# Performance work log

Hardware: AMD Instinct MI355X
Metric: run time of the kernel (lower is better)

The kernel has to match this reference:

```python
import jax, jax.numpy as jnp
import numpy as np

N_MASTER = 100000
N_BOND = 200000
N_GLOB = 5000
E1 = 400000
E2 = 100000
D_IN = 64
D_OUT = 64
H = 4
SLOPE = 0.2  # leaky relu negative slope


def _mlp(x, W0, b0, W1, b1, W2):
    # LinearN with num_fc_layers=3: ELU, ELU, Identity (last layer no bias)
    h = jax.nn.elu(x @ W0 + b0)
    h = jax.nn.elu(h @ W1 + b1)
    return h @ W2  # (N, H*D_OUT)


def setup_inputs() -> dict:
    key = jax.random.key(0)
    ks = jax.random.split(key, 32)
    s = 0.1  # weight scale
    d = {
        "master_feats": jax.random.normal(ks[0], (N_MASTER, D_IN), jnp.float32),
        "bond_feats": jax.random.normal(ks[1], (N_BOND, D_IN), jnp.float32),
        "global_feats": jax.random.normal(ks[2], (N_GLOB, D_IN), jnp.float32),
        "atom_W0": jax.random.normal(ks[3], (D_IN, D_OUT), jnp.float32) * s,
        "atom_b0": jnp.zeros((D_OUT,), jnp.float32),
        "atom_W1": jax.random.normal(ks[4], (D_OUT, D_OUT), jnp.float32) * s,
        "atom_b1": jnp.zeros((D_OUT,), jnp.float32),
        "atom_W2": jax.random.normal(ks[5], (D_OUT, H * D_OUT), jnp.float32) * s,
        "bond_W0": jax.random.normal(ks[6], (D_IN, D_OUT), jnp.float32) * s,
        "bond_b0": jnp.zeros((D_OUT,), jnp.float32),
        "bond_W1": jax.random.normal(ks[7], (D_OUT, D_OUT), jnp.float32) * s,
        "bond_b1": jnp.zeros((D_OUT,), jnp.float32),
        "bond_W2": jax.random.normal(ks[8], (D_OUT, H * D_OUT), jnp.float32) * s,
        "glob_W0": jax.random.normal(ks[9], (D_IN, D_OUT), jnp.float32) * s,
        "glob_b0": jnp.zeros((D_OUT,), jnp.float32),
        "glob_W1": jax.random.normal(ks[10], (D_OUT, D_OUT), jnp.float32) * s,
        "glob_b1": jnp.zeros((D_OUT,), jnp.float32),
        "glob_W2": jax.random.normal(ks[11], (D_OUT, H * D_OUT), jnp.float32) * s,
        "attn_l": jax.random.normal(ks[12], (H, D_OUT), jnp.float32) * s,
        "attn_r": jax.random.normal(ks[13], (H, D_OUT), jnp.float32) * s,
        "e1_src": jax.random.randint(ks[14], (E1,), 0, N_BOND, jnp.int32),
        "e1_dst": jax.random.randint(ks[15], (E1,), 0, N_MASTER, jnp.int32),
        "e2_src": jax.random.randint(ks[16], (E2,), 0, N_GLOB, jnp.int32),
        "e2_dst": jax.random.randint(ks[17], (E2,), 0, N_MASTER, jnp.int32),
    }
    return d


def reference(master_feats, bond_feats, global_feats,
              atom_W0, atom_b0, atom_W1, atom_b1, atom_W2,
              bond_W0, bond_b0, bond_W1, bond_b1, bond_W2,
              glob_W0, glob_b0, glob_W1, glob_b1, glob_W2,
              attn_l, attn_r, e1_src, e1_dst, e2_src, e2_dst):
    # Per-node-type projections to (N, H, D_OUT)
    ft_m = _mlp(master_feats, atom_W0, atom_b0, atom_W1, atom_b1, atom_W2).reshape(N_MASTER, H, D_OUT)
    ft_b = _mlp(bond_feats, bond_W0, bond_b0, bond_W1, bond_b1, bond_W2).reshape(N_BOND, H, D_OUT)
    ft_g = _mlp(global_feats, glob_W0, glob_b0, glob_W1, glob_b1, glob_W2).reshape(N_GLOB, H, D_OUT)

    er = jnp.einsum('nhd,hd->nh', ft_m, attn_r)  # master (dst) scores
    el_b = jnp.einsum('nhd,hd->nh', ft_b, attn_l)
    el_g = jnp.einsum('nhd,hd->nh', ft_g, attn_l)

    # Per-edge logits: u_add_v then leaky relu
    e1 = jax.nn.leaky_relu(el_b[e1_src] + er[e1_dst], negative_slope=SLOPE)  # (E1, H)
    e2 = jax.nn.leaky_relu(el_g[e2_src] + er[e2_dst], negative_slope=SLOPE)  # (E2, H)

    # Joint edge softmax over all incoming edges per master node
    dst_all = jnp.concatenate([e1_dst, e2_dst])  # (E1+E2,)
    e_all = jnp.concatenate([e1, e2], axis=0)    # (E1+E2, H)
    emax = jax.ops.segment_max(e_all, dst_all, num_segments=N_MASTER)  # (N, H)
    ex = jnp.exp(e_all - emax[dst_all])
    esum = jax.ops.segment_sum(ex, dst_all, num_segments=N_MASTER)     # (N, H)
    a = ex / esum[dst_all]                                             # (E, H)

    # Aggregate: u_mul_e, sum per destination master node
    src_ft = jnp.concatenate([ft_b[e1_src], ft_g[e2_src]], axis=0)     # (E, H, D)
    msgs = src_ft * a[:, :, None]
    rst = jax.ops.segment_sum(msgs, dst_all, num_segments=N_MASTER)    # (N, H, D)
    return rst
```

## Files before the change

kernel.cpp:

```cpp
#include <hip/hip_runtime.h>

#define NM 100000
#define NB 200000
#define NG 5000
#define NE1 400000
#define NE2 100000
#define NE (NE1 + NE2)
#define NMP 100004
#define SCAN_BLOCKS 391

typedef __attribute__((ext_vector_type(8))) short bf16x8;
typedef __attribute__((ext_vector_type(4))) short short4v;
typedef __attribute__((ext_vector_type(4))) float f32x4;

__device__ __forceinline__ unsigned short f2bf(float f) {
    unsigned int u = __float_as_uint(f);
    u += 0x7FFFu + ((u >> 16) & 1u);
    return (unsigned short)(u >> 16);
}
__device__ __forceinline__ float bf2f(unsigned short u) {
    return __uint_as_float((unsigned int)u << 16);
}
__device__ __forceinline__ float elu_f(float x) {
    return x > 0.f ? x : __expf(x) - 1.f;
}
__device__ __forceinline__ char* swz(char* base, int j, int byteoff) {
    return base + j * 128 + ((((byteoff >> 4) ^ (j & 7)) << 4) | (byteoff & 15));
}

struct WEnt { const float* W; short* o; int I; int off; };
struct WAll { WEnt e[9]; };

__global__ __launch_bounds__(256) void wprep_all_kernel(WAll a)
{
    const int idx = blockIdx.x * 256 + threadIdx.x;
    #pragma unroll
    for (int j = 8; j >= 0; --j) {
        if (idx >= a.e[j].off) {
            const int local = idx - a.e[j].off;
            const int I = a.e[j].I;
            const int i = local >> 6, k = local & 63;
            a.e[j].o[local] = (short)f2bf(a.e[j].W[k * I + i]);
            break;
        }
    }
}

__global__ __launch_bounds__(256) void mlp_mfma_kernel(
    const float* __restrict__ x, int N,
    const short* __restrict__ W0t, const float* __restrict__ b0,
    const short* __restrict__ W1t, const float* __restrict__ b1,
    const short* __restrict__ W2t,
    const float* __restrict__ attn,
    float* __restrict__ score,
    unsigned short* __restrict__ ft_out)
{
    __shared__ __attribute__((aligned(128))) char ldsA[64 * 128];
    __shared__ __attribute__((aligned(128))) char ldsB[64 * 128];

    const int tid = threadIdx.x;
    const int w = tid >> 6, l = tid & 63;
    const int g = l >> 4, c = l & 15;
    const int r0 = blockIdx.x << 6;

    {
        const int j = tid >> 2, q = tid & 3;
        const int row = r0 + j;
        bf16x8 o0 = (bf16x8)0, o1 = (bf16x8)0;
        if (row < N) {
            const float4* xp = (const float4*)(x + ((size_t)row << 6) + (q << 4));
            #pragma unroll
            for (int u = 0; u < 2; ++u) {
                float4 v = xp[u];
                o0[u*4+0] = (short)f2bf(v.x); o0[u*4+1] = (short)f2bf(v.y);
                o0[u*4+2] = (short)f2bf(v.z); o0[u*4+3] = (short)f2bf(v.w);
            }
            #pragma unroll
            for (int u = 0; u < 2; ++u) {
                float4 v = xp[u + 2];
                o1[u*4+0] = (short)f2bf(v.x); o1[u*4+1] = (short)f2bf(v.y);
                o1[u*4+2] = (short)f2bf(v.z); o1[u*4+3] = (short)f2bf(v.w);
            }
        }
        *(bf16x8*)swz(ldsA, j, q * 32)      = o0;
        *(bf16x8*)swz(ldsA, j, q * 32 + 16) = o1;
    }
    __syncthreads();

    char* src = ldsA;
    char* dst = ldsB;
    #pragma unroll
    for (int layer = 0; layer < 2; ++layer) {
        const short* Wt = layer ? W1t : W0t;
        const float* bb = layer ? b1 : b0;
        f32x4 acc[4] = {};
        #pragma unroll
        for (int step = 0; step < 2; ++step) {
            bf16x8 a = *(const bf16x8*)(Wt + (((16 * w + c) << 6) + 32 * step + 8 * g));
            #pragma unroll
            for (int t = 0; t < 4; ++t) {
                const int j = 16 * t + c;
                bf16x8 b = *(const bf16x8*)swz(src, j, 64 * step + 16 * g);
                acc[t] = __builtin_amdgcn_mfma_f32_16x16x32_bf16(a, b, acc[t], 0, 0, 0);
            }
        }
        const int i0 = 16 * w + 4 * g;
        const float4 bias = *(const float4*)(bb + i0);
        #pragma unroll
        for (int t = 0; t < 4; ++t) {
            const int j = 16 * t + c;
            short4v o;
            o[0] = (short)f2bf(elu_f(acc[t][0] + bias.x));
            o[1] = (short)f2bf(elu_f(acc[t][1] + bias.y));
            o[2] = (short)f2bf(elu_f(acc[t][2] + bias.z));
            o[3] = (short)f2bf(elu_f(acc[t][3] + bias.w));
            *(short4v*)swz(dst, j, 32 * w + 8 * g) = o;
        }
        __syncthreads();
        char* tmp = src; src = dst; dst = tmp;
    }

    {
        f32x4 acc[4][4] = {};
        #pragma unroll
        for (int step = 0; step < 2; ++step) {
            bf16x8 bfr[4];
            #pragma unroll
            for (int t = 0; t < 4; ++t)
                bfr[t] = *(const bf16x8*)swz(src, 16 * t + c, 64 * step + 16 * g);
            #pragma unroll
            for (int it = 0; it < 4; ++it) {
                bf16x8 a = *(const bf16x8*)(W2t + (((64 * w + 16 * it + c) << 6) + 32 * step + 8 * g));
                #pragma unroll
                for (int t = 0; t < 4; ++t)
                    acc[it][t] = __builtin_amdgcn_mfma_f32_16x16x32_bf16(a, bfr[t], acc[it][t], 0, 0, 0);
            }
        }
        float4 av[4];
        #pragma unroll
        for (int it = 0; it < 4; ++it)
            av[it] = *(const float4*)(attn + 64 * w + 16 * it + 4 * g);

        #pragma unroll
        for (int t = 0; t < 4; ++t) {
            const int row = r0 + 16 * t + c;
            float p = 0.f;
            #pragma unroll
            for (int it = 0; it < 4; ++it) {
                p += acc[it][t][0] * av[it].x + acc[it][t][1] * av[it].y
                   + acc[it][t][2] * av[it].z + acc[it][t][3] * av[it].w;
            }
            p += __shfl_xor(p, 16);
            p += __shfl_xor(p, 32);
            if (row < N) {
                if (g == 0) score[(row << 2) + w] = p;
                if (ft_out) {
                    #pragma unroll
                    for (int it = 0; it < 4; ++it) {
                        short4v o;
                        o[0] = (short)f2bf(acc[it][t][0]);
                        o[1] = (short)f2bf(acc[it][t][1]);
                        o[2] = (short)f2bf(acc[it][t][2]);
                        o[3] = (short)f2bf(acc[it][t][3]);
                        __builtin_nontemporal_store(o,
                            (short4v*)(ft_out + ((size_t)row << 8) + 64 * w + 16 * it + 4 * g));
                    }
                }
            }
        }
    }
}

__global__ void hist_kernel(const int* __restrict__ e1_dst,
                            const int* __restrict__ e2_dst,
                            int* __restrict__ counts)
{
    int i = blockIdx.x * blockDim.x + threadIdx.x;
    if (i < NE1) atomicAdd(&counts[e1_dst[i]], 1);
    else if (i < NE) atomicAdd(&counts[e2_dst[i - NE1]], 1);
}

__global__ __launch_bounds__(256) void scan1_kernel(
    const int* __restrict__ counts,
    int* __restrict__ prefix_inc,
    int* __restrict__ blocksums)
{
    const int i = blockIdx.x * 256 + threadIdx.x;
    const int lane = threadIdx.x & 63, wv = threadIdx.x >> 6;
    int v = (i < NM) ? counts[i] : 0;
    int x = v;
    #pragma unroll
    for (int o = 1; o < 64; o <<= 1) {
        int u = __shfl_up(x, o);
        if (lane >= o) x += u;
    }
    __shared__ int wsum[4];
    if (lane == 63) wsum[wv] = x;
    __syncthreads();
    int add = 0;
    #pragma unroll
    for (int k = 0; k < 3; ++k) add += (k < wv) ? wsum[k] : 0;
    x += add;
    if (i < NM) prefix_inc[i] = x;
    if (threadIdx.x == 255) blocksums[blockIdx.x] = x;
}

__global__ __launch_bounds__(512) void scan2_kernel(int* __restrict__ blocksums)
{
    const int t = threadIdx.x;
    const int lane = t & 63, wv = t >> 6;
    int v = (t < SCAN_BLOCKS) ? blocksums[t] : 0;
    int x = v;
    #pragma unroll
    for (int o = 1; o < 64; o <<= 1) {
        int u = __shfl_up(x, o);
        if (lane >= o) x += u;
    }
    __shared__ int wsum[8];
    if (lane == 63) wsum[wv] = x;
    __syncthreads();
    int add = 0;
    #pragma unroll
    for (int k = 0; k < 7; ++k) add += (k < wv) ? wsum[k] : 0;
    x += add;
    if (t < SCAN_BLOCKS) blocksums[t] = x - v;
}

__global__ __launch_bounds__(256) void scan3_kernel(
    const int* __restrict__ counts,
    const int* __restrict__ prefix_inc,
    const int* __restrict__ blocksums,
    int* __restrict__ offsets,
    int* __restrict__ cursor)
{
    const int i = blockIdx.x * 256 + threadIdx.x;
    if (i > NM) return;
    if (i == NM) { offsets[NM] = NE; return; }
    const int off = prefix_inc[i] - counts[i] + blocksums[blockIdx.x];
    offsets[i] = off;
    cursor[i]  = off;
}

__global__ void fill_kernel(const int* __restrict__ e1_src,
                            const int* __restrict__ e1_dst,
                            const int* __restrict__ e2_src,
                            const int* __restrict__ e2_dst,
                            const float* __restrict__ er,
                            const float* __restrict__ el_b,
                            const float* __restrict__ el_g,
                            int* __restrict__ cursor,
                            int* __restrict__ sorted,
                            float4* __restrict__ vsort)
{
    int i = blockIdx.x * blockDim.x + threadIdx.x;
    if (i >= NE) return;
    int dst, src, enc;
    const float* el;
    if (i < NE1) { src = e1_src[i]; dst = e1_dst[i]; enc = src;              el = el_b; }
    else { int j = i - NE1; src = e2_src[j]; dst = e2_dst[j]; enc = src | (1 << 30); el = el_g; }
    const float4 l4 = *(const float4*)(el + (src << 2));
    const float4 r4 = *(const float4*)(er + (dst << 2));
    float4 v;
    v.x = l4.x + r4.x; v.x = v.x > 0.f ? v.x : 0.2f * v.x;
    v.y = l4.y + r4.y; v.y = v.y > 0.f ? v.y : 0.2f * v.y;
    v.z = l4.z + r4.z; v.z = v.z > 0.f ? v.z : 0.2f * v.z;
    v.w = l4.w + r4.w; v.w = v.w > 0.f ? v.w : 0.2f * v.w;
    int p = atomicAdd(&cursor[dst], 1);
    sorted[p] = enc;
    vsort[p] = v;
}

__global__ __launch_bounds__(256) void aggregate_kernel(
    const int* __restrict__ offsets,
    const int* __restrict__ sorted,
    const float* __restrict__ vsort,
    const unsigned short* __restrict__ ftb,
    const unsigned short* __restrict__ ftg,
    float* __restrict__ out)
{
    const int w = threadIdx.x >> 6, l = threadIdx.x & 63;
    const int h  = l >> 4;
    const int f4 = l << 2;

    const int n = (blockIdx.x << 2) + w;
    if (n >= NM) return;

    const int start = offsets[n];
    const int deg   = offsets[n + 1] - start;

    f32x4 o = {};
    if (deg > 0) {
        int   encA = sorted[start];
        float vA   = vsort[(start << 2) + h];
        const int i1 = start + (deg > 1 ? 1 : 0);
        int   encB = sorted[i1];
        float vB   = vsort[(i1 << 2) + h];
        const unsigned short* pA =
            ((encA >> 30) ? ftg : ftb) + (((size_t)(encA & 0x3FFFFFFF)) << 8) + f4;
        short4v ftA = *(const short4v*)pA;

        float s = 0.f;
        for (int e = 0; e < deg; ++e) {
            const int i2 = start + min(e + 2, deg - 1);
            const int   encC = sorted[i2];
            const float vC   = vsort[(i2 << 2) + h];
            const unsigned short* pB =
                ((encB >> 30) ? ftg : ftb) + (((size_t)(encB & 0x3FFFFFFF)) << 8) + f4;
            const short4v ftB = *(const short4v*)pB;

            const float wgt = __expf(vA);
            s += wgt;
            o[0] = fmaf(bf2f((unsigned short)ftA[0]), wgt, o[0]);
            o[1] = fmaf(bf2f((unsigned short)ftA[1]), wgt, o[1]);
            o[2] = fmaf(bf2f((unsigned short)ftA[2]), wgt, o[2]);
            o[3] = fmaf(bf2f((unsigned short)ftA[3]), wgt, o[3]);

            ftA = ftB; vA = vB; encB = encC; vB = vC;
        }
        const float inv = 1.f / s;
        o[0] *= inv; o[1] *= inv; o[2] *= inv; o[3] *= inv;
    }
    __builtin_nontemporal_store(o, (f32x4*)(out + ((size_t)n << 8) + f4));
}

extern "C" void kernel_launch(void* const* d_in, const int* in_sizes, int n_in,
                              void* d_out, int out_size, void* d_ws, size_t ws_size,
                              hipStream_t stream)
{
    const float* master = (const float*)d_in[0];
    const float* bond   = (const float*)d_in[1];
    const float* glob   = (const float*)d_in[2];
    const float* aW0 = (const float*)d_in[3];
    const float* ab0 = (const float*)d_in[4];
    const float* aW1 = (const float*)d_in[5];
    const float* ab1 = (const float*)d_in[6];
    const float* aW2 = (const float*)d_in[7];
    const float* bW0 = (const float*)d_in[8];
    const float* bb0 = (const float*)d_in[9];
    const float* bW1 = (const float*)d_in[10];
    const float* bb1 = (const float*)d_in[11];
    const float* bW2 = (const float*)d_in[12];
    const float* gW0 = (const float*)d_in[13];
    const float* gb0 = (const float*)d_in[14];
    const float* gW1 = (const float*)d_in[15];
    const float* gb1 = (const float*)d_in[16];
    const float* gW2 = (const float*)d_in[17];
    const float* attn_l = (const float*)d_in[18];
    const float* attn_r = (const float*)d_in[19];
    const int* e1_src = (const int*)d_in[20];
    const int* e1_dst = (const int*)d_in[21];
    const int* e2_src = (const int*)d_in[22];
    const int* e2_dst = (const int*)d_in[23];
    float* out = (float*)d_out;

    float* ws   = (float*)d_ws;
    unsigned short* ft_b = (unsigned short*)ws;
    unsigned short* ft_g = ft_b + (size_t)NB * 256;
    float* er   = (float*)(ft_g + (size_t)NG * 256);
    float* el_b = er + (size_t)NM * 4;
    float* el_g = el_b + (size_t)NB * 4;
    int* counts  = (int*)(el_g + (size_t)NG * 4);
    int* offsets = counts + NMP;
    int* cursor  = offsets + NMP;
    int* sorted  = cursor + NMP;
    float4* vsort = (float4*)(sorted + NE);
    int* prefix_inc = (int*)(vsort + NE);
    int* blocksums  = prefix_inc + NMP;
    short* wtA = (short*)(blocksums + 512);
    short* wtB = wtA + 24576;
    short* wtG = wtB + 24576;

    hipMemsetAsync(counts, 0, sizeof(int) * NM, stream);

    WAll wa;
    wa.e[0] = {aW0, wtA,          64,     0};
    wa.e[1] = {aW1, wtA + 4096,   64,  4096};
    wa.e[2] = {aW2, wtA + 8192,  256,  8192};
    wa.e[3] = {bW0, wtB,          64, 24576};
    wa.e[4] = {bW1, wtB + 4096,   64, 28672};
    wa.e[5] = {bW2, wtB + 8192,  256, 32768};
    wa.e[6] = {gW0, wtG,          64, 49152};
    wa.e[7] = {gW1, wtG + 4096,   64, 53248};
    wa.e[8] = {gW2, wtG + 8192,  256, 57344};
    wprep_all_kernel<<<288, 256, 0, stream>>>(wa);

    mlp_mfma_kernel<<<(NM + 63) / 64, 256, 0, stream>>>(
        master, NM, wtA, ab0, wtA + 4096, ab1, wtA + 8192, attn_r, er, nullptr);
    mlp_mfma_kernel<<<(NB + 63) / 64, 256, 0, stream>>>(
        bond, NB, wtB, bb0, wtB + 4096, bb1, wtB + 8192, attn_l, el_b, ft_b);
    mlp_mfma_kernel<<<(NG + 63) / 64, 256, 0, stream>>>(
        glob, NG, wtG, gb0, wtG + 4096, gb1, wtG + 8192, attn_l, el_g, ft_g);

    hist_kernel<<<(NE + 255) / 256, 256, 0, stream>>>(e1_dst, e2_dst, counts);
    scan1_kernel<<<SCAN_BLOCKS, 256, 0, stream>>>(counts, prefix_inc, blocksums);
    scan2_kernel<<<1, 512, 0, stream>>>(blocksums);
    scan3_kernel<<<SCAN_BLOCKS + 1, 256, 0, stream>>>(counts, prefix_inc, blocksums,
                                                      offsets, cursor);
    fill_kernel<<<(NE + 255) / 256, 256, 0, stream>>>(e1_src, e1_dst, e2_src, e2_dst,
                                                      er, el_b, el_g,
                                                      cursor, sorted, vsort);
    aggregate_kernel<<<(NM + 3) / 4, 256, 0, stream>>>(offsets, sorted,
                                                       (const float*)vsort,
                                                       ft_b, ft_g, out);
}
```

Measured before the change: 236.6 us.

## Batch edge gathers per wave with cooperative index loads and shuffles

The aggregate kernel now has each wave load up to 16 edge indices and logits cooperatively, one per lane, and broadcast them with shuffles. It then issues all 16 feature-row gathers before doing any FMA, so many loads are in flight at once instead of one edge at a time through a short software prefetch. Bond and global feature tables are addressed as a single contiguous array (global rows offset by NB), which removes the per-edge table select. The cost is higher register use for the 16-entry buffer and some wasted work on low-degree nodes; this relies on ft_g sitting directly after ft_b in the workspace.

Result: faster. 223.2 us (-5.7%).

```diff
diff --git a/kernel.cpp b/kernel.cpp
--- a/kernel.cpp
+++ b/kernel.cpp
@@ -249,15 +249,15 @@
                             const float* __restrict__ el_b,
                             const float* __restrict__ el_g,
                             int* __restrict__ cursor,
-                            int* __restrict__ sorted,
+                            int* __restrict__ rows,
                             float4* __restrict__ vsort)
 {
     int i = blockIdx.x * blockDim.x + threadIdx.x;
     if (i >= NE) return;
-    int dst, src, enc;
+    int dst, src, row;
     const float* el;
-    if (i < NE1) { src = e1_src[i]; dst = e1_dst[i]; enc = src;              el = el_b; }
-    else { int j = i - NE1; src = e2_src[j]; dst = e2_dst[j]; enc = src | (1 << 30); el = el_g; }
+    if (i < NE1) { src = e1_src[i]; dst = e1_dst[i]; row = src;      el = el_b; }
+    else { int j = i - NE1; src = e2_src[j]; dst = e2_dst[j]; row = NB + src; el = el_g; }
     const float4 l4 = *(const float4*)(el + (src << 2));
     const float4 r4 = *(const float4*)(er + (dst << 2));
     float4 v;
@@ -266,21 +266,21 @@
     v.z = l4.z + r4.z; v.z = v.z > 0.f ? v.z : 0.2f * v.z;
     v.w = l4.w + r4.w; v.w = v.w > 0.f ? v.w : 0.2f * v.w;
     int p = atomicAdd(&cursor[dst], 1);
-    sorted[p] = enc;
+    rows[p] = row;
     vsort[p] = v;
 }
 
 __global__ __launch_bounds__(256) void aggregate_kernel(
     const int* __restrict__ offsets,
-    const int* __restrict__ sorted,
+    const int* __restrict__ rows,
     const float* __restrict__ vsort,
-    const unsigned short* __restrict__ ftb,
-    const unsigned short* __restrict__ ftg,
+    const unsigned short* __restrict__ ft,
     float* __restrict__ out)
 {
     const int w = threadIdx.x >> 6, l = threadIdx.x & 63;
-    const int h  = l >> 4;
-    const int f4 = l << 2;
+    const int h   = l >> 4;
+    const int e16 = l & 15;
+    const int f4  = l << 2;
 
     const int n = (blockIdx.x << 2) + w;
     if (n >= NM) return;
@@ -289,34 +289,36 @@
     const int deg   = offsets[n + 1] - start;
 
     f32x4 o = {};
+    float s = 0.f;
+    for (int b = 0; b < deg; b += 16) {
+        const int rem = min(deg - b, 16);
+        int   row_l = 0;
+        float v_l   = 0.f;
+        if (e16 < rem) {
+            row_l = rows[start + b + e16];
+            v_l   = vsort[((start + b + e16) << 2) + h];
+        }
+        short4v ftv[16];
+        #pragma unroll
+        for (int e = 0; e < 16; ++e) {
+            if (e < rem) {
+                const int row = __shfl(row_l, e);
+                ftv[e] = *(const short4v*)(ft + ((size_t)row << 8) + f4);
+            }
+        }
+        #pragma unroll
+        for (int e = 0; e < 16; ++e) {
+            if (e < rem) {
+                const float wgt = __expf(__shfl(v_l, (h << 4) + e));
+                s += wgt;
+                o[0] = fmaf(bf2f((unsigned short)ftv[e][0]), wgt, o[0]);
+                o[1] = fmaf(bf2f((unsigned short)ftv[e][1]), wgt, o[1]);
+                o[2] = fmaf(bf2f((unsigned short)ftv[e][2]), wgt, o[2]);
+                o[3] = fmaf(bf2f((unsigned short)ftv[e][3]), wgt, o[3]);
+            }
+        }
+    }
     if (deg > 0) {
-        int   encA = sorted[start];
-        float vA   = vsort[(start << 2) + h];
-        const int i1 = start + (deg > 1 ? 1 : 0);
-        int   encB = sorted[i1];
-        float vB   = vsort[(i1 << 2) + h];
-        const unsigned short* pA =
-            ((encA >> 30) ? ftg : ftb) + (((size_t)(encA & 0x3FFFFFFF)) << 8) + f4;
-        short4v ftA = *(const short4v*)pA;
-
-        float s = 0.f;
-        for (int e = 0; e < deg; ++e) {
-            const int i2 = start + min(e + 2, deg - 1);
-            const int   encC = sorted[i2];
-            const float vC   = vsort[(i2 << 2) + h];
-            const unsigned short* pB =
-                ((encB >> 30) ? ftg : ftb) + (((size_t)(encB & 0x3FFFFFFF)) << 8) + f4;
-            const short4v ftB = *(const short4v*)pB;
-
-            const float wgt = __expf(vA);
-            s += wgt;
-            o[0] = fmaf(bf2f((unsigned short)ftA[0]), wgt, o[0]);
-            o[1] = fmaf(bf2f((unsigned short)ftA[1]), wgt, o[1]);
-            o[2] = fmaf(bf2f((unsigned short)ftA[2]), wgt, o[2]);
-            o[3] = fmaf(bf2f((unsigned short)ftA[3]), wgt, o[3]);
-
-            ftA = ftB; vA = vB; encB = encC; vB = vC;
-        }
         const float inv = 1.f / s;
         o[0] *= inv; o[1] *= inv; o[2] *= inv; o[3] *= inv;
     }
@@ -362,8 +364,8 @@
     int* counts  = (int*)(el_g + (size_t)NG * 4);
     int* offsets = counts + NMP;
     int* cursor  = offsets + NMP;
-    int* sorted  = cursor + NMP;
-    float4* vsort = (float4*)(sorted + NE);
+    int* rows    = cursor + NMP;
+    float4* vsort = (float4*)(rows + NE);
     int* prefix_inc = (int*)(vsort + NE);
     int* blocksums  = prefix_inc + NMP;
     short* wtA = (short*)(blocksums + 512);
@@ -398,8 +400,8 @@
                                                       offsets, cursor);
     fill_kernel<<<(NE + 255) / 256, 256, 0, stream>>>(e1_src, e1_dst, e2_src, e2_dst,
                                                       er, el_b, el_g,
-                                                      cursor, sorted, vsort);
-    aggregate_kernel<<<(NM + 3) / 4, 256, 0, stream>>>(offsets, sorted,
+                                                      cursor, rows, vsort);
+    aggregate_kernel<<<(NM + 3) / 4, 256, 0, stream>>>(offsets, rows,
                                                        (const float*)vsort,
-                                                       ft_b, ft_g, out);
-}
+                                                       ft_b, out);
+}
```
